# Performance work log

Hardware: AMD Instinct MI355X
Metric: run time of the kernel (lower is better)

The kernel has to match this reference:

```python
import jax, jax.numpy as jnp
import numpy as np

EPS = 1e-05  # matches tf entropy epsilon


def setup_inputs() -> dict:
    key = jax.random.key(0)
    k1, k2 = jax.random.split(key)
    encodings = jax.random.normal(k1, (8192, 64), dtype=jnp.float32)
    categorical = jax.random.uniform(k2, (8192, 25), dtype=jnp.float32)
    return {"encodings": encodings, "categorical": categorical, "k": 15}


def reference(encodings, categorical, k):
    B = encodings.shape[0]
    n_components = categorical.shape[1]
    k = min(k, B // 4)  # layer clamps k to batch_size // 4

    hard_groups = jnp.argmax(categorical, axis=1)           # [B] int
    max_groups = jnp.max(categorical, axis=1)               # [B]

    # Batched brute-force kNN. tf.norm's sqrt is monotonic, so the strict
    # comparison `dist < kth_dist` is identical on squared distances; working
    # in squared space avoids sqrt(0) issues and an extra pass.
    sq = jnp.sum(encodings * encodings, axis=1)             # [B]
    d2 = sq[:, None] + sq[None, :] - 2.0 * (encodings @ encodings.T)
    d2 = jnp.maximum(d2, 0.0)                               # [B, B]

    # (k+1)-smallest distances per row (0-indexed k, self-distance included,
    # matching tf.gather(tf.sort(distances), k)).
    neg_topk, _ = jax.lax.top_k(-d2, k + 1)                 # [B, k+1]
    kth = -neg_topk[:, k]                                   # [B] k-th smallest

    mask = (d2 < kth[:, None]).astype(jnp.float32)          # [B, B] strict <

    # Per-row label histogram over the neighborhood: counts[i,c] = #neighbors
    # of i in cluster c. Zero bins contribute 0 to -sum(b*log(b+eps)), same as
    # tf.bincount's variable-length output.
    onehot = jax.nn.one_hot(hard_groups, n_components, dtype=jnp.float32)
    counts = mask @ onehot                                  # [B, n_components]
    n_i = jnp.sum(counts, axis=-1, keepdims=True)           # [B, 1]
    bins = counts / jnp.maximum(n_i, 1.0)
    neighbourhood_entropy = -jnp.sum(bins * jnp.log(bins + EPS), axis=-1)  # [B]

    # Global cluster-size entropy + number of populated clusters.
    gcounts = jnp.sum(onehot, axis=0)                       # [n_components]
    gbins = gcounts / jnp.float32(B)
    cluster_size_entropy = -jnp.sum(gbins * jnp.log(gbins + EPS))
    n_populated = jnp.sum(gcounts > 0).astype(jnp.float32)

    return encodings, neighbourhood_entropy, cluster_size_entropy, n_populated, max_groups
```

## Files before the change

### kernel.cpp

```cpp
#include <hip/hip_runtime.h>
#include <math.h>

#define Bsz    8192
#define Dd     64
#define NC     25
#define RT     32
#define KCAP   16
#define EPSf   1e-5f
#define JMASK  2097151
#define SENT   0x7FFFFFFF

typedef short  short8  __attribute__((ext_vector_type(8)));
typedef float  floatx4 __attribute__((ext_vector_type(4)));


__device__ inline unsigned short f2bf(float x) {
    unsigned u = __float_as_uint(x);
    u += 0x7FFFu + ((u >> 16) & 1u);
    return (unsigned short)(u >> 16);
}
__device__ inline float bf2f(unsigned short h) { return __uint_as_float(((unsigned)h) << 16); }

__device__ inline void oesort16(int* a) {
    #pragma unroll
    for (int p = 1; p < 16; p <<= 1) {
        #pragma unroll
        for (int k = p; k >= 1; k >>= 1) {
            #pragma unroll
            for (int j = (k & (p - 1)); j + k < 16; j += 2 * k) {
                #pragma unroll
                for (int i = 0; i < k; ++i) {
                    if (i + j + k < 16 &&
                        ((i + j) / (2 * p)) == ((i + j + k) / (2 * p))) {
                        int x = a[i + j], y = a[i + j + k];
                        a[i + j]     = (x < y) ? x : y;
                        a[i + j + k] = (x < y) ? y : x;
                    }
                }
            }
        }
    }
}
__device__ inline void bclean16(int* t) {
    #pragma unroll
    for (int j = 8; j > 0; j >>= 1)
        #pragma unroll
        for (int i = 0; i < 16; ++i) {
            int l = i ^ j;
            if (l > i) {
                int x = t[i], y = t[l];
                t[i] = (x < y) ? x : y;
                t[l] = (x < y) ? y : x;
            }
        }
}
__device__ inline void bmerge16(int* ls, const int* b) {
    int t[16];
    #pragma unroll
    for (int i = 0; i < 16; ++i) { int x = ls[i], y = b[15 - i]; t[i] = (x < y) ? x : y; }
    bclean16(t);
    #pragma unroll
    for (int i = 0; i < 16; ++i) ls[i] = t[i];
}
__device__ inline void bmerge16_shfl(int* ls, int mask) {
    int t[16];
    #pragma unroll
    for (int i = 0; i < 16; ++i) {
        int pv = __shfl_xor(ls[15 - i], mask);
        int x = ls[i];
        t[i] = (x < pv) ? x : pv;
    }
    bclean16(t);
    #pragma unroll
    for (int i = 0; i < 16; ++i) ls[i] = t[i];
}

struct TileR { short8 a0, a1, a2, a3; uint4 sv; };

__device__ __attribute__((always_inline)) inline void tile_load(
    TileR& T, const char* __restrict__ enc2, const unsigned* __restrict__ slab,
    int soff, int lane16, int quad4)
{
    const char* base = enc2 + soff + lane16;
    T.a0 = *(const short8*)(base);
    T.a1 = *(const short8*)(base + 1024);
    T.a2 = *(const short8*)(base + 2048);
    T.a3 = *(const short8*)(base + 3072);
    T.sv = *(const uint4*)(slab + (soff >> 8) + quad4);
}

__device__ __attribute__((always_inline)) inline void tile_mfma2(
    const TileR& T,
    const short8* bh0, const short8* bl0, const short8* bh1, const short8* bl1,
    float sqi0, float sqi1, int* c0, int* c1)
{
    floatx4 p = (floatx4){0.f, 0.f, 0.f, 0.f};
    floatx4 q = (floatx4){0.f, 0.f, 0.f, 0.f};
    p = __builtin_amdgcn_mfma_f32_16x16x32_bf16(T.a0, bh0[0], p, 0, 0, 0);
    q = __builtin_amdgcn_mfma_f32_16x16x32_bf16(T.a0, bh1[0], q, 0, 0, 0);
    p = __builtin_amdgcn_mfma_f32_16x16x32_bf16(T.a0, bl0[0], p, 0, 0, 0);
    q = __builtin_amdgcn_mfma_f32_16x16x32_bf16(T.a0, bl1[0], q, 0, 0, 0);
    p = __builtin_amdgcn_mfma_f32_16x16x32_bf16(T.a2, bh0[0], p, 0, 0, 0);
    q = __builtin_amdgcn_mfma_f32_16x16x32_bf16(T.a2, bh1[0], q, 0, 0, 0);
    p = __builtin_amdgcn_mfma_f32_16x16x32_bf16(T.a1, bh0[1], p, 0, 0, 0);
    q = __builtin_amdgcn_mfma_f32_16x16x32_bf16(T.a1, bh1[1], q, 0, 0, 0);
    p = __builtin_amdgcn_mfma_f32_16x16x32_bf16(T.a1, bl0[1], p, 0, 0, 0);
    q = __builtin_amdgcn_mfma_f32_16x16x32_bf16(T.a1, bl1[1], q, 0, 0, 0);
    p = __builtin_amdgcn_mfma_f32_16x16x32_bf16(T.a3, bh0[1], p, 0, 0, 0);
    q = __builtin_amdgcn_mfma_f32_16x16x32_bf16(T.a3, bh1[1], q, 0, 0, 0);

    const unsigned s4[4] = {T.sv.x, T.sv.y, T.sv.z, T.sv.w};
    #pragma unroll
    for (int r = 0; r < 4; ++r) {
        const unsigned sqb = s4[r] & ~31u, lb = s4[r] & 31u;
        float d0 = sqi0 + __uint_as_float(sqb) + p[r];
        c0[r] = (int)((__float_as_uint(d0) & ~31u) | lb);
        float d1 = sqi1 + __uint_as_float(sqb) + q[r];
        c1[r] = (int)((__float_as_uint(d1) & ~31u) | lb);
    }
}


__global__ __launch_bounds__(256) void pre_kernel(
    const float* __restrict__ enc, const float* __restrict__ cat,
    unsigned int* __restrict__ slab,
    char* __restrict__ enc1, char* __restrict__ enc2,
    float* __restrict__ out_max, float* __restrict__ out_enc)
{
    const int gid = blockIdx.x * 256 + threadIdx.x;
    const int p = gid >> 5, pr = gid & 31;

    float2 ev = ((const float2*)enc)[gid];
    ((float2*)out_enc)[gid] = ev;

    float s = ev.x * ev.x + ev.y * ev.y;
    #pragma unroll
    for (int m = 1; m < 32; m <<= 1) s += __shfl_xor(s, m, 32);

    {
        const int g = p >> 4, c15p = p & 15;
        const int d0 = 2 * pr, kh = d0 >> 5, q = (d0 >> 3) & 3, e0 = d0 & 7;
        const int base = g * 4096 + kh * 1024 + (q * 16 + c15p) * 16 + e0 * 2;
        unsigned short ha = f2bf(ev.x), hb = f2bf(ev.y);
        unsigned short la = f2bf(ev.x - bf2f(ha)), lb = f2bf(ev.y - bf2f(hb));
        *(unsigned*)(enc1 + base)        = (unsigned)ha | ((unsigned)hb << 16);
        *(unsigned*)(enc1 + base + 2048) = (unsigned)la | ((unsigned)lb << 16);
        float y0 = -2.f * ev.x, y1 = -2.f * ev.y;
        unsigned short hc = f2bf(y0), hd = f2bf(y1);
        unsigned short lc = f2bf(y0 - bf2f(hc)), ld = f2bf(y1 - bf2f(hd));
        *(unsigned*)(enc2 + base)        = (unsigned)hc | ((unsigned)hd << 16);
        *(unsigned*)(enc2 + base + 2048) = (unsigned)lc | ((unsigned)ld << 16);
    }
    float cv = (pr < NC) ? cat[p * NC + pr] : -1.f;
    int ci = pr;
    #pragma unroll
    for (int m = 1; m < 32; m <<= 1) {
        float ov = __shfl_xor(cv, m, 32);
        int   oi = __shfl_xor(ci, m, 32);
        if (ov > cv || (ov == cv && oi < ci)) { cv = ov; ci = oi; }
    }
    if (pr == 0) {
        out_max[p] = cv;
        slab[p] = (__float_as_uint(s) & ~31u) | (unsigned)ci;
    }
}

__global__ __launch_bounds__(512) void main_kernel(
    const char* __restrict__ enc1, const char* __restrict__ enc2,
    const unsigned int* __restrict__ slab, const int* __restrict__ kptr,
    float* __restrict__ out_ent, float* __restrict__ out_glob)
{
    __shared__ int wl[8 * 32 * 17];
    __shared__ int cnt[32];

    const int tid  = threadIdx.x, bid = blockIdx.x;
    const int wv   = tid >> 6, lane = tid & 63;
    const int quad = (tid >> 4) & 3, c15 = tid & 15;
    const int rowbase = bid * RT;
    const int lane16 = lane * 16, quad4 = quad * 4;

    short8 bh0[2], bl0[2], bh1[2], bl1[2];
    {
        const char* ib = enc1 + (size_t)bid * 8192 + lane16;
        bh0[0] = *(const short8*)(ib);
        bh0[1] = *(const short8*)(ib + 1024);
        bl0[0] = *(const short8*)(ib + 2048);
        bl0[1] = *(const short8*)(ib + 3072);
        bh1[0] = *(const short8*)(ib + 4096);
        bh1[1] = *(const short8*)(ib + 5120);
        bl1[0] = *(const short8*)(ib + 6144);
        bl1[1] = *(const short8*)(ib + 7168);
    }
    const float sqi0 = __uint_as_float(slab[rowbase + c15] & ~31u);
    const float sqi1 = __uint_as_float(slab[rowbase + 16 + c15] & ~31u);

    int ls0[KCAP], ls1[KCAP];
    #pragma unroll
    for (int q = 0; q < KCAP; ++q) { ls0[q] = SENT; ls1[q] = SENT; }

    const int wvoff = wv * 4096;

    TileR A0, A1, B0, B1;
    tile_load(A0, enc2, slab, wvoff,          lane16, quad4);
    tile_load(A1, enc2, slab, wvoff + 32768,  lane16, quad4);

    #pragma unroll 1
    for (int p = 0; p < 32; p += 2) {
        int c0[16], c1[16];
        {
            const int o = (wvoff + (p + 1) * 65536) & JMASK;
            tile_load(B0, enc2, slab, o, lane16, quad4);
        }
        __builtin_amdgcn_sched_barrier(0);
        tile_mfma2(A0, bh0, bl0, bh1, bl1, sqi0, sqi1, c0, c1);
        {
            const int o = ((wvoff + (p + 1) * 65536) & JMASK) + 32768;
            tile_load(B1, enc2, slab, o, lane16, quad4);
        }
        __builtin_amdgcn_sched_barrier(0);
        tile_mfma2(A1, bh0, bl0, bh1, bl1, sqi0, sqi1, c0 + 4, c1 + 4);
        {
            const int o = (wvoff + (p + 2) * 65536) & JMASK;
            tile_load(A0, enc2, slab, o, lane16, quad4);
        }
        __builtin_amdgcn_sched_barrier(0);
        tile_mfma2(B0, bh0, bl0, bh1, bl1, sqi0, sqi1, c0 + 8, c1 + 8);
        {
            const int o = ((wvoff + (p + 2) * 65536) & JMASK) + 32768;
            tile_load(A1, enc2, slab, o, lane16, quad4);
        }
        __builtin_amdgcn_sched_barrier(0);
        tile_mfma2(B1, bh0, bl0, bh1, bl1, sqi0, sqi1, c0 + 12, c1 + 12);
        oesort16(c0);
        bmerge16(ls0, c0);
        oesort16(c1);
        bmerge16(ls1, c1);
    }

    if (bid == 0) {
        if (tid < 32) cnt[tid] = 0;
        __syncthreads();
        for (int i = tid; i < Bsz; i += 512) atomicAdd(&cnt[slab[i] & 31u], 1);
        __syncthreads();
        if (tid == 0) {
            float gent = 0.f, npop = 0.f;
            for (int i = 0; i < NC; ++i) {
                int g = cnt[i];
                if (g > 0) {
                    npop += 1.f;
                    float gb = (float)g / (float)Bsz;
                    gent -= gb * logf(gb + EPSf);
                }
            }
            out_glob[0] = gent;
            out_glob[1] = npop;
        }
        __syncthreads();
    }

    bmerge16_shfl(ls0, 16);
    bmerge16_shfl(ls0, 32);
    bmerge16_shfl(ls1, 16);
    bmerge16_shfl(ls1, 32);
    if (quad == 0) {
        #pragma unroll
        for (int q = 0; q < KCAP; ++q) wl[(wv * 32 + c15) * 17 + q]      = ls0[q];
        #pragma unroll
        for (int q = 0; q < KCAP; ++q) wl[(wv * 32 + 16 + c15) * 17 + q] = ls1[q];
    }
    __syncthreads();
    if (wv < 2) {
        const int row = tid >> 2, sub = tid & 3;
        int A[16], Bv[16];
        #pragma unroll
        for (int i = 0; i < 16; ++i) A[i]  = wl[((2 * sub)     * 32 + row) * 17 + i];
        #pragma unroll
        for (int i = 0; i < 16; ++i) Bv[i] = wl[((2 * sub + 1) * 32 + row) * 17 + i];
        bmerge16(A, Bv);
        bmerge16_shfl(A, 1);
        bmerge16_shfl(A, 2);

        int kk = kptr[0];
        if (kk > Bsz / 4) kk = Bsz / 4;
        if (kk > KCAP - 1) kk = KCAP - 1;

        int kth = A[15];
        #pragma unroll
        for (int q = 0; q < 16; ++q) if (q == kk) kth = A[q];
        int nn = 0;
        #pragma unroll
        for (int t = 0; t < 15; ++t) nn += (t < kk && A[t] < kth) ? 1 : 0;

        float inv = 1.f / (float)((nn > 0) ? nn : 1);
        float part = 0.f;
        #pragma unroll
        for (int a4 = 0; a4 < 4; ++a4) {
            int a = sub + 4 * a4;
            if (a < nn) {
                int la = A[a] & 31;
                int c = 0;
                #pragma unroll
                for (int b = 0; b < 15; ++b) c += (b < nn && (A[b] & 31) == la) ? 1 : 0;
                part -= inv * logf((float)c * inv + EPSf);
            }
        }
        part += __shfl_xor(part, 1);
        part += __shfl_xor(part, 2);
        if (sub == 0) out_ent[rowbase + row] = part;
    }
}

extern "C" void kernel_launch(void* const* d_in, const int* in_sizes, int n_in,
                              void* d_out, int out_size, void* d_ws, size_t ws_size,
                              hipStream_t stream)
{
    const float* enc  = (const float*)d_in[0];
    const float* cat  = (const float*)d_in[1];
    const int*   kptr = (const int*)d_in[2];
    float* out = (float*)d_out;

    unsigned int* slab = (unsigned int*)d_ws;
    char*         enc1 = (char*)d_ws + 32768;
    char*         enc2 = (char*)d_ws + 2129920;

    float* out_enc  = out;
    float* out_ent  = out + Bsz * Dd;
    float* out_glob = out + Bsz * Dd + Bsz;
    float* out_max  = out + Bsz * Dd + Bsz + 2;

    pre_kernel<<<1024, 256, 0, stream>>>(enc, cat, slab, enc1, enc2, out_max, out_enc);
    main_kernel<<<Bsz / RT, 512, 0, stream>>>(enc1, enc2, slab, kptr, out_ent, out_glob);
}
```

Measured before the change: 111.1 us.

## Interleave 8-wide top-k sort/merge with MFMA tiles in software pipeline

Replaces the per-iteration 16-element sort and full 16x16 bitonic merge with 8-element batches that are sorted and merged one step behind the MFMA tile that produced them. The sort/merge work now sits between tile loads and MFMA issues, so VALU work can overlap matrix and memory latency. The cheaper merge only compares the upper half of the running list against the new batch. It adds extra live registers (a0/a1/b0/b1) and needs an epilogue to drain the last batch, which may raise register pressure.

New measurement: 115.2 us. +3.7%, slower.

```diff
diff --git a/kernel.cpp b/kernel.cpp
--- a/kernel.cpp
+++ b/kernel.cpp
@@ -21,16 +21,16 @@
 }
 __device__ inline float bf2f(unsigned short h) { return __uint_as_float(((unsigned)h) << 16); }
 
-__device__ inline void oesort16(int* a) {
-    #pragma unroll
-    for (int p = 1; p < 16; p <<= 1) {
+__device__ inline void oesort8(int* a) {
+    #pragma unroll
+    for (int p = 1; p < 8; p <<= 1) {
         #pragma unroll
         for (int k = p; k >= 1; k >>= 1) {
             #pragma unroll
-            for (int j = (k & (p - 1)); j + k < 16; j += 2 * k) {
+            for (int j = (k & (p - 1)); j + k < 8; j += 2 * k) {
                 #pragma unroll
                 for (int i = 0; i < k; ++i) {
-                    if (i + j + k < 16 &&
+                    if (i + j + k < 8 &&
                         ((i + j) / (2 * p)) == ((i + j + k) / (2 * p))) {
                         int x = a[i + j], y = a[i + j + k];
                         a[i + j]     = (x < y) ? x : y;
@@ -53,6 +53,16 @@
                 t[l] = (x < y) ? y : x;
             }
         }
+}
+__device__ inline void bmerge16_8(int* ls, const int* c) {
+    int t[16];
+    #pragma unroll
+    for (int i = 0; i < 8; ++i) t[i] = ls[i];
+    #pragma unroll
+    for (int m = 0; m < 8; ++m) { int x = ls[8 + m], y = c[7 - m]; t[8 + m] = (x < y) ? x : y; }
+    bclean16(t);
+    #pragma unroll
+    for (int i = 0; i < 16; ++i) ls[i] = t[i];
 }
 __device__ inline void bmerge16(int* ls, const int* b) {
     int t[16];
@@ -200,42 +210,42 @@
 
     const int wvoff = wv * 4096;
 
+    int a0[8], a1[8], b0[8], b1[8];
+    #pragma unroll
+    for (int q = 0; q < 8; ++q) { b0[q] = SENT; b1[q] = SENT; }
+
     TileR A0, A1, B0, B1;
     tile_load(A0, enc2, slab, wvoff,          lane16, quad4);
     tile_load(A1, enc2, slab, wvoff + 32768,  lane16, quad4);
 
     #pragma unroll 1
-    for (int p = 0; p < 32; p += 2) {
-        int c0[16], c1[16];
-        {
-            const int o = (wvoff + (p + 1) * 65536) & JMASK;
-            tile_load(B0, enc2, slab, o, lane16, quad4);
-        }
+    for (int u = 0; u < 16; ++u) {
+        const int base = wvoff + u * 131072;
+        tile_load(B0, enc2, slab, (base + 65536) & JMASK, lane16, quad4);
         __builtin_amdgcn_sched_barrier(0);
-        tile_mfma2(A0, bh0, bl0, bh1, bl1, sqi0, sqi1, c0, c1);
-        {
-            const int o = ((wvoff + (p + 1) * 65536) & JMASK) + 32768;
-            tile_load(B1, enc2, slab, o, lane16, quad4);
-        }
+        tile_mfma2(A0, bh0, bl0, bh1, bl1, sqi0, sqi1, a0, a1);
+        oesort8(b0);
+        bmerge16_8(ls0, b0);
+        tile_load(B1, enc2, slab, (base + 98304) & JMASK, lane16, quad4);
         __builtin_amdgcn_sched_barrier(0);
-        tile_mfma2(A1, bh0, bl0, bh1, bl1, sqi0, sqi1, c0 + 4, c1 + 4);
-        {
-            const int o = (wvoff + (p + 2) * 65536) & JMASK;
-            tile_load(A0, enc2, slab, o, lane16, quad4);
-        }
+        tile_mfma2(A1, bh0, bl0, bh1, bl1, sqi0, sqi1, a0 + 4, a1 + 4);
+        oesort8(b1);
+        bmerge16_8(ls1, b1);
+        tile_load(A0, enc2, slab, (base + 131072) & JMASK, lane16, quad4);
         __builtin_amdgcn_sched_barrier(0);
-        tile_mfma2(B0, bh0, bl0, bh1, bl1, sqi0, sqi1, c0 + 8, c1 + 8);
-        {
-            const int o = ((wvoff + (p + 2) * 65536) & JMASK) + 32768;
-            tile_load(A1, enc2, slab, o, lane16, quad4);
-        }
+        tile_mfma2(B0, bh0, bl0, bh1, bl1, sqi0, sqi1, b0, b1);
+        oesort8(a0);
+        bmerge16_8(ls0, a0);
+        tile_load(A1, enc2, slab, (base + 163840) & JMASK, lane16, quad4);
         __builtin_amdgcn_sched_barrier(0);
-        tile_mfma2(B1, bh0, bl0, bh1, bl1, sqi0, sqi1, c0 + 12, c1 + 12);
-        oesort16(c0);
-        bmerge16(ls0, c0);
-        oesort16(c1);
-        bmerge16(ls1, c1);
-    }
+        tile_mfma2(B1, bh0, bl0, bh1, bl1, sqi0, sqi1, b0 + 4, b1 + 4);
+        oesort8(a1);
+        bmerge16_8(ls1, a1);
+    }
+    oesort8(b0);
+    bmerge16_8(ls0, b0);
+    oesort8(b1);
+    bmerge16_8(ls1, b1);
 
     if (bid == 0) {
         if (tid < 32) cnt[tid] = 0;
```
